# Optimization experiments

Measured on AMD Instinct MI355X. Metric: run time of the kernel, lower is better.

The kernel has to match this reference:

```python
import jax, jax.numpy as jnp
import numpy as np

N_NODES = 100000
N_EDGES = 1600000
D = 128
LEAKY_ALPHA = 0.2
ELU_ALPHA = 1.0


def setup_inputs() -> dict:
    key = jax.random.key(0)
    ks = jax.random.split(key, 8)
    s = 0.05
    atom_features = jax.random.normal(ks[0], (N_NODES, D), dtype=jnp.float32)
    W1 = jax.random.normal(ks[1], (1, 2 * D), dtype=jnp.float32) * s
    b1 = jnp.zeros((1,), dtype=jnp.float32)
    W2 = jax.random.normal(ks[2], (D, D), dtype=jnp.float32) * s
    b2 = jnp.zeros((D,), dtype=jnp.float32)
    w_ih = jax.random.normal(ks[3], (3 * D, D), dtype=jnp.float32) * s
    w_hh = jax.random.normal(ks[4], (3 * D, D), dtype=jnp.float32) * s
    b_ih = jnp.zeros((3 * D,), dtype=jnp.float32)
    b_hh = jnp.zeros((3 * D,), dtype=jnp.float32)
    edge_index = jax.random.randint(ks[5], (2, N_EDGES), 0, N_NODES, dtype=jnp.int64)
    return {"atom_features": atom_features, "W1": W1, "b1": b1, "W2": W2,
            "b2": b2, "w_ih": w_ih, "w_hh": w_hh, "b_ih": b_ih, "b_hh": b_hh,
            "edge_index": edge_index}


def _elu(x, alpha):
    return jnp.where(x > 0, x, alpha * (jnp.exp(jnp.minimum(x, 0.0)) - 1.0))


def reference(atom_features, W1, b1, W2, b2, w_ih, w_hh, b_ih, b_hh, edge_index):
    N, d = atom_features.shape
    src = edge_index[0]  # neighbor j (keys[0])
    dst = edge_index[1]  # center node i (keys[1])

    # atom_fc2 transform (dropout is identity in eval)
    nft = atom_features @ W2.T + b2  # [N, d]

    # attention logit per edge: leaky_relu(W1 @ concat(h_dst, h_src) + b1)
    w_d = W1[0, :d]
    w_s = W1[0, d:]
    logit = atom_features @ w_d  # [N]
    logit_src = atom_features @ w_s  # [N]
    score = logit[dst] + logit_src[src] + b1[0]  # [E]
    score = jnp.where(score > 0, score, LEAKY_ALPHA * score)

    # segment softmax over incoming edges of each dst node
    m = jax.ops.segment_max(score, dst, num_segments=N)  # -inf for isolated nodes
    m_safe = jnp.where(jnp.isfinite(m), m, 0.0)
    e = jnp.exp(score - m_safe[dst])  # [E]
    denom = jax.ops.segment_sum(e, dst, num_segments=N)  # [N]
    attn = e / denom[dst]  # [E]

    # weighted scatter-sum of transformed neighbor features
    msg = attn[:, None] * nft[src]  # [E, d]
    transform = jax.ops.segment_sum(msg, dst, num_segments=N)  # [N, d]
    context = _elu(transform, ELU_ALPHA)

    deg = jax.ops.segment_sum(jnp.ones_like(score), dst, num_segments=N)
    out_emb = jnp.where(deg[:, None] > 0, context, atom_features)

    # GRUCell(out_emb, atom_features): torch gate ordering r, z, n
    gi = out_emb @ w_ih.T + b_ih  # [N, 3d]
    gh = atom_features @ w_hh.T + b_hh  # [N, 3d]
    gi_r, gi_z, gi_n = jnp.split(gi, 3, axis=-1)
    gh_r, gh_z, gh_n = jnp.split(gh, 3, axis=-1)
    r = jax.nn.sigmoid(gi_r + gh_r)
    z = jax.nn.sigmoid(gi_z + gh_z)
    n = jnp.tanh(gi_n + r * gh_n)
    h_new = (1.0 - z) * n + z * atom_features
    return h_new
```

## Files before the change

kernel.cpp:

```cpp
#include <hip/hip_runtime.h>
#include <cstdint>
#include <cstddef>

#define D 128
#define LEAKY_ALPHA 0.2f

#define BSHIFT 8
#define BCAP 4608
#define NBUK_MAX 512

typedef __attribute__((ext_vector_type(8))) short short8;
typedef __attribute__((ext_vector_type(4))) short short4v;
typedef __attribute__((ext_vector_type(4))) float f32x4;
typedef __attribute__((ext_vector_type(2))) float f32x2;

static __device__ __forceinline__ unsigned short f32_to_bf16_rne(float v) {
  unsigned x = __float_as_uint(v);
  unsigned r = (x + 0x7fffu + ((x >> 16) & 1u)) >> 16;
  return (unsigned short)r;
}
static __device__ __forceinline__ float bf16_to_f32(unsigned short u) {
  return __uint_as_float(((unsigned)u) << 16);
}

#if __has_builtin(__builtin_amdgcn_cvt_pk_f32_fp8) && __has_builtin(__builtin_amdgcn_cvt_pk_fp8_f32)
#define FP8_HW 1
#endif

static __device__ __forceinline__ unsigned char f32_to_fp8(float x) {
#ifdef FP8_HW
  return (unsigned char)(__builtin_amdgcn_cvt_pk_fp8_f32(x, x, 0, false) & 0xff);
#else
  unsigned u = __float_as_uint(x);
  unsigned s = (u >> 24) & 0x80u;
  unsigned mag = u & 0x7fffffffu;
  if (mag == 0) return (unsigned char)s;
  int e = (int)(mag >> 23) - 127;
  unsigned full = (mag & 0x7fffffu) | 0x800000u;
  if (e >= 9) return (unsigned char)(s | 0x7Eu);
  int sh = (e >= -6) ? 20 : 20 + (-6 - e);
  if (sh > 24) return (unsigned char)s;
  unsigned keep = full >> sh;
  unsigned rem = full & ((1u << sh) - 1u);
  unsigned half = 1u << (sh - 1);
  if (rem > half || (rem == half && (keep & 1u))) keep++;
  unsigned em;
  if (e >= -6) {
    unsigned v = ((unsigned)(e + 7) << 3) + keep - 8u;
    if (v > 0x7Eu) v = 0x7Eu;
    em = v;
  } else {
    em = keep;
  }
  return (unsigned char)(s | em);
#endif
}

#ifndef FP8_HW
static __device__ __forceinline__ float fp8_dec(unsigned b) {
  unsigned em = b & 0x7fu, s = (b & 0x80u) << 24;
  float m;
  if (em >= 8) m = __uint_as_float(0x3C000000u + (em << 20));
  else m = (float)em * 0.001953125f;
  return __uint_as_float(s | __float_as_uint(m));
}
#endif

static __device__ __forceinline__ void fp8_fma16(uint4 u, float e, float* acc) {
#ifdef FP8_HW
  f32x2 t;
  t = __builtin_amdgcn_cvt_pk_f32_fp8(u.x, false); acc[0] += e*t[0]; acc[1] += e*t[1];
  t = __builtin_amdgcn_cvt_pk_f32_fp8(u.x, true ); acc[2] += e*t[0]; acc[3] += e*t[1];
  t = __builtin_amdgcn_cvt_pk_f32_fp8(u.y, false); acc[4] += e*t[0]; acc[5] += e*t[1];
  t = __builtin_amdgcn_cvt_pk_f32_fp8(u.y, true ); acc[6] += e*t[0]; acc[7] += e*t[1];
  t = __builtin_amdgcn_cvt_pk_f32_fp8(u.z, false); acc[8] += e*t[0]; acc[9] += e*t[1];
  t = __builtin_amdgcn_cvt_pk_f32_fp8(u.z, true ); acc[10]+= e*t[0]; acc[11]+= e*t[1];
  t = __builtin_amdgcn_cvt_pk_f32_fp8(u.w, false); acc[12]+= e*t[0]; acc[13]+= e*t[1];
  t = __builtin_amdgcn_cvt_pk_f32_fp8(u.w, true ); acc[14]+= e*t[0]; acc[15]+= e*t[1];
#else
  unsigned ws[4] = {u.x, u.y, u.z, u.w};
  #pragma unroll
  for (int k = 0; k < 4; ++k)
    #pragma unroll
    for (int b = 0; b < 4; ++b)
      acc[k * 4 + b] += e * fp8_dec((ws[k] >> (8 * b)) & 0xffu);
#endif
}

__global__ __launch_bounds__(256) void k_wprep(
    const float* __restrict__ W1, const float* __restrict__ W2,
    const float* __restrict__ w_ih, const float* __restrict__ w_hh,
    unsigned short* __restrict__ Wcat, unsigned short* __restrict__ Wb) {
  int idx = blockIdx.x * 256 + threadIdx.x;
  if (idx < 144 * 128) {
    int r = idx >> 7, c = idx & 127;
    float v = 0.f;
    if (r < 128)      v = W2[r * 128 + c];
    else if (r == 128) v = W1[c];
    else if (r == 129) v = W1[128 + c];
    Wcat[idx] = f32_to_bf16_rne(v);
    return;
  }
  int i2 = idx - 144 * 128;
  if (i2 < 384 * 256) {
    int r = i2 >> 8, c = i2 & 255;
    float v = (c < D) ? w_ih[r * D + c] : w_hh[r * D + (c - D)];
    Wb[i2] = f32_to_bf16_rne(v);
  }
}

#define NPITCH 136
__global__ __launch_bounds__(256, 2) void k_front(
    const float* __restrict__ A, const unsigned short* __restrict__ Wcat,
    const float* __restrict__ b2, unsigned char* __restrict__ nftb,
    float* __restrict__ logit_d, float* __restrict__ logit_s,
    unsigned short* __restrict__ X,
    const int* __restrict__ ei, unsigned* __restrict__ cursors,
    unsigned* __restrict__ part,
    int N, int E, int NBUK, int EPB, int nftBlocks) {
  __shared__ short sA[64 * NPITCH];
  __shared__ int hist[NBUK_MAX];
  __shared__ int sbase[NBUK_MAX];
  int tid = threadIdx.x;

  if ((int)blockIdx.x >= nftBlocks) {
    int t = tid;
    int pb = blockIdx.x - nftBlocks;
    int e0 = pb * EPB;
    int e1 = min(e0 + EPB, E);
    for (int i = t; i < NBUK; i += 256) hist[i] = 0;
    __syncthreads();
    for (int e = e0 + t; e < e1; e += 256)
      atomicAdd(&hist[ei[E + e] >> BSHIFT], 1);
    __syncthreads();
    for (int i = t; i < NBUK; i += 256) {
      int h = hist[i];
      sbase[i] = h ? (int)atomicAdd(&cursors[i * 16], (unsigned)h) : 0;
      hist[i] = 0;
    }
    __syncthreads();
    for (int e = e0 + t; e < e1; e += 256) {
      int src = ei[e];
      int dst = ei[E + e];
      int b = dst >> BSHIFT;
      int lp = sbase[b] + atomicAdd(&hist[b], 1);
      if (lp < BCAP)
        part[(size_t)b * BCAP + lp] =
            ((unsigned)(dst & ((1 << BSHIFT) - 1)) << 24) | (unsigned)src;
    }
    return;
  }

  int n0 = blockIdx.x * 64;

  #pragma unroll
  for (int i = 0; i < 8; ++i) {
    int g = i * 1024 + tid * 4;
    int row = g >> 7, col = g & 127;
    int gr = n0 + row; if (gr >= N) gr = N - 1;
    float4 v = *(const float4*)&A[(size_t)gr * D + col];
    short4v b;
    b.x = (short)f32_to_bf16_rne(v.x);
    b.y = (short)f32_to_bf16_rne(v.y);
    b.z = (short)f32_to_bf16_rne(v.z);
    b.w = (short)f32_to_bf16_rne(v.w);
    *(short4v*)&sA[row * NPITCH + col] = b;
  }
  __syncthreads();

  int w = tid >> 6, lane = tid & 63, l15 = lane & 15, l4 = lane >> 4;

  f32x4 acc[4][2], acc8[4];
  #pragma unroll
  for (int rt = 0; rt < 4; ++rt) {
    acc[rt][0] = (f32x4)0.f; acc[rt][1] = (f32x4)0.f; acc8[rt] = (f32x4)0.f;
  }

  #pragma unroll
  for (int ks = 0; ks < 4; ++ks) {
    int kk = ks * 32 + l4 * 8;
    short8 a[4];
    #pragma unroll
    for (int rt = 0; rt < 4; ++rt)
      a[rt] = *(const short8*)&sA[(rt * 16 + l15) * NPITCH + kk];
    short8 b0 = *(const short8*)&Wcat[(size_t)(w * 16 + l15) * 128 + kk];
    short8 b1 = *(const short8*)&Wcat[(size_t)((w + 4) * 16 + l15) * 128 + kk];
    #pragma unroll
    for (int rt = 0; rt < 4; ++rt) {
      acc[rt][0] = __builtin_amdgcn_mfma_f32_16x16x32_bf16(a[rt], b0, acc[rt][0], 0, 0, 0);
      acc[rt][1] = __builtin_amdgcn_mfma_f32_16x16x32_bf16(a[rt], b1, acc[rt][1], 0, 0, 0);
    }
    if (w == 0) {
      short8 b2v = *(const short8*)&Wcat[(size_t)(128 + l15) * 128 + kk];
      #pragma unroll
      for (int rt = 0; rt < 4; ++rt)
        acc8[rt] = __builtin_amdgcn_mfma_f32_16x16x32_bf16(a[rt], b2v, acc8[rt], 0, 0, 0);
    }
  }

  #pragma unroll
  for (int i = 0; i < 4; ++i) {
    int g = i * 2048 + tid * 8;
    int row = g >> 7, col = g & 127;
    if (n0 + row < N) {
      short8 v = *(const short8*)&sA[row * NPITCH + col];
      *(short8*)&X[(size_t)(n0 + row) * 256 + 128 + col] = v;
    }
  }

  #pragma unroll
  for (int t = 0; t < 2; ++t) {
    int j = (w + 4 * t) * 16 + l15;
    float bb = b2[j];
    #pragma unroll
    for (int rt = 0; rt < 4; ++rt)
      #pragma unroll
      for (int jr = 0; jr < 4; ++jr) {
        int row = n0 + rt * 16 + l4 * 4 + jr;
        if (row < N)
          nftb[(size_t)row * D + j] = f32_to_fp8(acc[rt][t][jr] + bb);
      }
  }
  if (w == 0 && l15 < 2) {
    float* dst = (l15 == 0) ? logit_d : logit_s;
    #pragma unroll
    for (int rt = 0; rt < 4; ++rt)
      #pragma unroll
      for (int jr = 0; jr < 4; ++jr) {
        int row = n0 + rt * 16 + l4 * 4 + jr;
        if (row < N) dst[row] = acc8[rt][jr];
      }
  }
}

__global__ __launch_bounds__(256) void k_bucket_csr(
    const unsigned* __restrict__ cursors, const unsigned* __restrict__ part,
    const float* __restrict__ logit_d, const float* __restrict__ logit_s,
    const float* __restrict__ b1, uint2* __restrict__ rec,
    int2* __restrict__ beg_end, int N) {
  __shared__ unsigned ents[BCAP];
  __shared__ int hist[256];
  __shared__ int scn[256];
  __shared__ int cur[256];
  __shared__ float sld[256];
  int b = blockIdx.x, t = threadIdx.x;
  int nb0 = b << BSHIFT;
  int cnt = (int)cursors[b * 16];
  if (cnt > BCAP) cnt = BCAP;
  hist[t] = 0;
  {
    int n = nb0 + t;
    sld[t] = (n < N) ? logit_d[n] + b1[0] : 0.f;
  }
  __syncthreads();
  const unsigned* reg = part + (size_t)b * BCAP;
  uint2* rrec = rec + (size_t)b * BCAP;
  for (int i = t; i < cnt; i += 256) {
    unsigned p = reg[i];
    ents[i] = p;
    atomicAdd(&hist[p >> 24], 1);
  }
  __syncthreads();
  int v = hist[t];
  scn[t] = v;
  __syncthreads();
  for (int o = 1; o < 256; o <<= 1) {
    int x = (t >= o) ? scn[t - o] : 0;
    __syncthreads();
    scn[t] += x;
    __syncthreads();
  }
  int excl = scn[t] - v;
  cur[t] = excl;
  int n = nb0 + t;
  if (n < N) beg_end[n] = make_int2(b * BCAP + excl, b * BCAP + excl + v);
  __syncthreads();
  for (int i = t; i < cnt; i += 256) {
    unsigned p = ents[i];
    int dl = p >> 24;
    int lp = atomicAdd(&cur[dl], 1);
    unsigned s = p & 0xFFFFFFu;
    float sc = sld[dl] + logit_s[s];
    sc = sc > 0.f ? sc : LEAKY_ALPHA * sc;
    rrec[lp] = make_uint2(s, __float_as_uint(__expf(sc)));
  }
}

#define XPITCH 264
__global__ __launch_bounds__(512, 1) void k_gat_gru(
    const int2* __restrict__ beg_end, const uint2* __restrict__ rec,
    const unsigned char* __restrict__ nftb,
    const unsigned short* X,
    const unsigned short* __restrict__ Wb,
    const float* __restrict__ b_ih, const float* __restrict__ b_hh,
    float* out, int N) {
  __shared__ short sX[64 * XPITCH];
  int tid = threadIdx.x;
  int n0 = blockIdx.x * 64;

  #pragma unroll
  for (int i = 0; i < 2; ++i) {
    int idx = i * 512 + tid;
    int row = idx >> 4, c8 = idx & 15;
    int gr = n0 + row; if (gr >= N) gr = N - 1;
    short8 v = *(const short8*)&X[(size_t)gr * 256 + 128 + c8 * 8];
    *(short8*)&sX[row * XPITCH + 128 + c8 * 8] = v;
  }
  __syncthreads();

  {
    int l  = tid & 7;
    int nl = tid >> 3;
    int n  = n0 + nl;
    short8 xo0, xo1;
    if (n < N) {
      int2 be = beg_end[n];
      int start = be.x, end = be.y;
      if (end == start) {
        xo0 = *(const short8*)&sX[nl * XPITCH + 128 + l * 16];
        xo1 = *(const short8*)&sX[nl * XPITCH + 128 + l * 16 + 8];
      } else {
        float acc[16];
        #pragma unroll
        for (int j = 0; j < 16; ++j) acc[j] = 0.f;
        float den = 0.f;
        int p = start;
        for (; p + 4 <= end; p += 4) {
          uint2 r0 = rec[p], r1 = rec[p + 1], r2 = rec[p + 2], r3 = rec[p + 3];
          uint4 u0 = *(const uint4*)&nftb[(size_t)r0.x * D + l * 16];
          uint4 u1 = *(const uint4*)&nftb[(size_t)r1.x * D + l * 16];
          uint4 u2 = *(const uint4*)&nftb[(size_t)r2.x * D + l * 16];
          uint4 u3 = *(const uint4*)&nftb[(size_t)r3.x * D + l * 16];
          float w0 = __uint_as_float(r0.y), w1 = __uint_as_float(r1.y);
          float w2 = __uint_as_float(r2.y), w3 = __uint_as_float(r3.y);
          den += (w0 + w1) + (w2 + w3);
          fp8_fma16(u0, w0, acc);
          fp8_fma16(u1, w1, acc);
          fp8_fma16(u2, w2, acc);
          fp8_fma16(u3, w3, acc);
        }
        for (; p < end; ++p) {
          uint2 r = rec[p];
          uint4 u = *(const uint4*)&nftb[(size_t)r.x * D + l * 16];
          float w0 = __uint_as_float(r.y);
          den += w0;
          fp8_fma16(u, w0, acc);
        }
        float inv = 1.f / den;
        #pragma unroll
        for (int j = 0; j < 16; ++j) {
          float t = acc[j] * inv;
          float oe = t > 0.f ? t : (__expf(t) - 1.f);
          if (j < 8) xo0[j] = (short)f32_to_bf16_rne(oe);
          else       xo1[j - 8] = (short)f32_to_bf16_rne(oe);
        }
      }
    } else {
      xo0 = (short8)0; xo1 = (short8)0;
    }
    *(short8*)&sX[nl * XPITCH + l * 16]     = xo0;
    *(short8*)&sX[nl * XPITCH + l * 16 + 8] = xo1;
  }
  __syncthreads();

  int w    = tid >> 6;
  int lane = tid & 63;
  int l15  = lane & 15;
  int l4   = lane >> 4;
  int j    = w * 16 + l15;

  f32x4 acc[4][4];
  #pragma unroll
  for (int rt = 0; rt < 4; ++rt)
    #pragma unroll
    for (int q = 0; q < 4; ++q) acc[rt][q] = (f32x4)0.f;

  #pragma unroll
  for (int ks = 0; ks < 8; ++ks) {
    int kk = ks * 32 + l4 * 8;
    short8 a[4];
    #pragma unroll
    for (int rt = 0; rt < 4; ++rt)
      a[rt] = *(const short8*)&sX[(rt * 16 + l15) * XPITCH + kk];
    short8 b0 = *(const short8*)&Wb[(size_t)(j) * 256 + kk];
    short8 b1 = *(const short8*)&Wb[(size_t)(128 + j) * 256 + kk];
    short8 b2 = *(const short8*)&Wb[(size_t)(256 + j) * 256 + kk];
    int qn = (ks < 4) ? 2 : 3;
    #pragma unroll
    for (int rt = 0; rt < 4; ++rt) {
      acc[rt][0]  = __builtin_amdgcn_mfma_f32_16x16x32_bf16(a[rt], b0, acc[rt][0], 0, 0, 0);
      acc[rt][1]  = __builtin_amdgcn_mfma_f32_16x16x32_bf16(a[rt], b1, acc[rt][1], 0, 0, 0);
      acc[rt][qn] = __builtin_amdgcn_mfma_f32_16x16x32_bf16(a[rt], b2, acc[rt][qn], 0, 0, 0);
    }
  }

  float br  = b_ih[j] + b_hh[j];
  float bz  = b_ih[D + j] + b_hh[D + j];
  float bin = b_ih[2 * D + j];
  float bhn = b_hh[2 * D + j];
  #pragma unroll
  for (int rt = 0; rt < 4; ++rt) {
    #pragma unroll
    for (int jr = 0; jr < 4; ++jr) {
      int lrow = rt * 16 + l4 * 4 + jr;
      int row = n0 + lrow;
      if (row < N) {
        float rp  = acc[rt][0][jr] + br;
        float zp  = acc[rt][1][jr] + bz;
        float gin = acc[rt][2][jr] + bin;
        float ghn = acc[rt][3][jr] + bhn;
        float r = 1.f / (1.f + __expf(-rp));
        float z = 1.f / (1.f + __expf(-zp));
        float t = gin + r * ghn;
        float e2 = __expf(2.f * t);
        float nn = 1.f - 2.f / (e2 + 1.f);
        float h = bf16_to_f32((unsigned short)sX[lrow * XPITCH + 128 + j]);
        out[(size_t)row * D + j] = (1.f - z) * nn + z * h;
      }
    }
  }
}

extern "C" void kernel_launch(void* const* d_in, const int* in_sizes, int n_in,
                              void* d_out, int out_size, void* d_ws, size_t ws_size,
                              hipStream_t stream) {
  const float* A    = (const float*)d_in[0];
  const float* W1   = (const float*)d_in[1];
  const float* b1   = (const float*)d_in[2];
  const float* W2   = (const float*)d_in[3];
  const float* b2   = (const float*)d_in[4];
  const float* w_ih = (const float*)d_in[5];
  const float* w_hh = (const float*)d_in[6];
  const float* b_ih = (const float*)d_in[7];
  const float* b_hh = (const float*)d_in[8];
  const int*   ei   = (const int*)d_in[9];

  int N = in_sizes[0] / D;
  int E = in_sizes[9] / 2;
  float* out = (float*)d_out;

  int NBUK = (N + (1 << BSHIFT) - 1) >> BSHIFT;

  char* ws = (char*)d_ws;
  unsigned char* nftb = (unsigned char*)ws;
  float* logit_d = (float*)(ws + (size_t)N * D);
  float* logit_s = logit_d + N;
  int2*  beg_end = (int2*)(logit_s + N);
  unsigned* cursors = (unsigned*)(beg_end + N);
  unsigned* part = cursors + (size_t)NBUK * 16;
  uint2* rec = (uint2*)(part + (size_t)NBUK * BCAP);
  unsigned short* Wb   = (unsigned short*)(rec + (size_t)NBUK * BCAP);
  unsigned short* Wcat = Wb + 384 * 256;

  hipMemsetAsync(cursors, 0, (size_t)NBUK * 16 * sizeof(unsigned), stream);

  k_wprep<<<(144 * 128 + 384 * 256 + 255) / 256, 256, 0, stream>>>(
      W1, W2, w_ih, w_hh, Wcat, Wb);

  int nftBlocks = (N + 63) / 64;
  int gridPart = 160;
  int EPB = (E + gridPart - 1) / gridPart;
  k_front<<<nftBlocks + gridPart, 256, 0, stream>>>(
      A, Wcat, b2, nftb, logit_d, logit_s, (unsigned short*)d_out,
      ei, cursors, part, N, E, NBUK, EPB, nftBlocks);

  k_bucket_csr<<<NBUK, 256, 0, stream>>>(cursors, part, logit_d, logit_s, b1,
                                         rec, beg_end, N);
  k_gat_gru<<<nftBlocks, 512, 0, stream>>>(beg_end, rec, nftb,
                                           (const unsigned short*)d_out,
                                           Wb, b_ih, b_hh, out, N);
}
```

Baseline: 191.8 us.

## Fuse bucket CSR build into GAT/GRU kernel with 64-node buckets

```diff
diff --git a/kernel.cpp b/kernel.cpp
--- a/kernel.cpp
+++ b/kernel.cpp
@@ -5,9 +5,9 @@
 #define D 128
 #define LEAKY_ALPHA 0.2f
 
-#define BSHIFT 8
-#define BCAP 4608
-#define NBUK_MAX 512
+#define BSHIFT 6
+#define BCAP 1344
+#define NBUK_MAX 2048
 
 typedef __attribute__((ext_vector_type(8))) short short8;
 typedef __attribute__((ext_vector_type(4))) short short4v;
@@ -90,7 +90,8 @@
 __global__ __launch_bounds__(256) void k_wprep(
     const float* __restrict__ W1, const float* __restrict__ W2,
     const float* __restrict__ w_ih, const float* __restrict__ w_hh,
-    unsigned short* __restrict__ Wcat, unsigned short* __restrict__ Wb) {
+    unsigned short* __restrict__ Wcat, unsigned short* __restrict__ Wb,
+    unsigned* __restrict__ cursors, int ncur) {
   int idx = blockIdx.x * 256 + threadIdx.x;
   if (idx < 144 * 128) {
     int r = idx >> 7, c = idx & 127;
@@ -106,7 +107,10 @@
     int r = i2 >> 8, c = i2 & 255;
     float v = (c < D) ? w_ih[r * D + c] : w_hh[r * D + (c - D)];
     Wb[i2] = f32_to_bf16_rne(v);
-  }
+    return;
+  }
+  int i3 = i2 - 384 * 256;
+  if (i3 < ncur) cursors[i3] = 0;
 }
 
 #define NPITCH 136
@@ -233,70 +237,27 @@
   }
 }
 
-__global__ __launch_bounds__(256) void k_bucket_csr(
+#define XPITCH 264
+__global__ __launch_bounds__(512, 1) void k_gat_gru(
     const unsigned* __restrict__ cursors, const unsigned* __restrict__ part,
     const float* __restrict__ logit_d, const float* __restrict__ logit_s,
-    const float* __restrict__ b1, uint2* __restrict__ rec,
-    int2* __restrict__ beg_end, int N) {
-  __shared__ unsigned ents[BCAP];
-  __shared__ int hist[256];
-  __shared__ int scn[256];
-  __shared__ int cur[256];
-  __shared__ float sld[256];
-  int b = blockIdx.x, t = threadIdx.x;
-  int nb0 = b << BSHIFT;
-  int cnt = (int)cursors[b * 16];
-  if (cnt > BCAP) cnt = BCAP;
-  hist[t] = 0;
-  {
-    int n = nb0 + t;
-    sld[t] = (n < N) ? logit_d[n] + b1[0] : 0.f;
-  }
-  __syncthreads();
-  const unsigned* reg = part + (size_t)b * BCAP;
-  uint2* rrec = rec + (size_t)b * BCAP;
-  for (int i = t; i < cnt; i += 256) {
-    unsigned p = reg[i];
-    ents[i] = p;
-    atomicAdd(&hist[p >> 24], 1);
-  }
-  __syncthreads();
-  int v = hist[t];
-  scn[t] = v;
-  __syncthreads();
-  for (int o = 1; o < 256; o <<= 1) {
-    int x = (t >= o) ? scn[t - o] : 0;
-    __syncthreads();
-    scn[t] += x;
-    __syncthreads();
-  }
-  int excl = scn[t] - v;
-  cur[t] = excl;
-  int n = nb0 + t;
-  if (n < N) beg_end[n] = make_int2(b * BCAP + excl, b * BCAP + excl + v);
-  __syncthreads();
-  for (int i = t; i < cnt; i += 256) {
-    unsigned p = ents[i];
-    int dl = p >> 24;
-    int lp = atomicAdd(&cur[dl], 1);
-    unsigned s = p & 0xFFFFFFu;
-    float sc = sld[dl] + logit_s[s];
-    sc = sc > 0.f ? sc : LEAKY_ALPHA * sc;
-    rrec[lp] = make_uint2(s, __float_as_uint(__expf(sc)));
-  }
-}
-
-#define XPITCH 264
-__global__ __launch_bounds__(512, 1) void k_gat_gru(
-    const int2* __restrict__ beg_end, const uint2* __restrict__ rec,
+    const float* __restrict__ b1,
     const unsigned char* __restrict__ nftb,
     const unsigned short* X,
     const unsigned short* __restrict__ Wb,
     const float* __restrict__ b_ih, const float* __restrict__ b_hh,
     float* out, int N) {
   __shared__ short sX[64 * XPITCH];
+  __shared__ unsigned ents[BCAP];
+  __shared__ uint2 srec[BCAP];
+  __shared__ int sbeg[64], scnt[64], cur[64];
+  __shared__ float sld[64];
   int tid = threadIdx.x;
-  int n0 = blockIdx.x * 64;
+  int b   = blockIdx.x;
+  int n0  = b * 64;
+
+  int cnt = (int)cursors[b * 16];
+  if (cnt > BCAP) cnt = BCAP;
 
   #pragma unroll
   for (int i = 0; i < 2; ++i) {
@@ -306,6 +267,41 @@
     short8 v = *(const short8*)&X[(size_t)gr * 256 + 128 + c8 * 8];
     *(short8*)&sX[row * XPITCH + 128 + c8 * 8] = v;
   }
+  for (int i = tid; i < cnt; i += 512) ents[i] = part[(size_t)b * BCAP + i];
+  if (tid < 64) {
+    int n = n0 + tid;
+    sld[tid] = (n < N) ? logit_d[n] + b1[0] : 0.f;
+    scnt[tid] = 0;
+  }
+  __syncthreads();
+
+  for (int i = tid; i < cnt; i += 512)
+    atomicAdd(&scnt[ents[i] >> 24], 1);
+  __syncthreads();
+
+  if (tid < 64) {
+    int v = scnt[tid];
+    int incl = v;
+    #pragma unroll
+    for (int o = 1; o < 64; o <<= 1) {
+      int x = __shfl_up(incl, o);
+      if (tid >= o) incl += x;
+    }
+    int excl = incl - v;
+    sbeg[tid] = excl;
+    cur[tid]  = excl;
+  }
+  __syncthreads();
+
+  for (int i = tid; i < cnt; i += 512) {
+    unsigned p = ents[i];
+    int dl = p >> 24;
+    unsigned s = p & 0xFFFFFFu;
+    int lp = atomicAdd(&cur[dl], 1);
+    float sc = sld[dl] + logit_s[s];
+    sc = sc > 0.f ? sc : LEAKY_ALPHA * sc;
+    srec[lp] = make_uint2(s, __float_as_uint(__expf(sc)));
+  }
   __syncthreads();
 
   {
@@ -314,8 +310,8 @@
     int n  = n0 + nl;
     short8 xo0, xo1;
     if (n < N) {
-      int2 be = beg_end[n];
-      int start = be.x, end = be.y;
+      int start = sbeg[nl];
+      int end   = start + scnt[nl];
       if (end == start) {
         xo0 = *(const short8*)&sX[nl * XPITCH + 128 + l * 16];
         xo1 = *(const short8*)&sX[nl * XPITCH + 128 + l * 16 + 8];
@@ -326,7 +322,7 @@
         float den = 0.f;
         int p = start;
         for (; p + 4 <= end; p += 4) {
-          uint2 r0 = rec[p], r1 = rec[p + 1], r2 = rec[p + 2], r3 = rec[p + 3];
+          uint2 r0 = srec[p], r1 = srec[p + 1], r2 = srec[p + 2], r3 = srec[p + 3];
           uint4 u0 = *(const uint4*)&nftb[(size_t)r0.x * D + l * 16];
           uint4 u1 = *(const uint4*)&nftb[(size_t)r1.x * D + l * 16];
           uint4 u2 = *(const uint4*)&nftb[(size_t)r2.x * D + l * 16];
@@ -340,7 +336,7 @@
           fp8_fma16(u3, w3, acc);
         }
         for (; p < end; ++p) {
-          uint2 r = rec[p];
+          uint2 r = srec[p];
           uint4 u = *(const uint4*)&nftb[(size_t)r.x * D + l * 16];
           float w0 = __uint_as_float(r.y);
           den += w0;
@@ -445,17 +441,15 @@
   unsigned char* nftb = (unsigned char*)ws;
   float* logit_d = (float*)(ws + (size_t)N * D);
   float* logit_s = logit_d + N;
-  int2*  beg_end = (int2*)(logit_s + N);
-  unsigned* cursors = (unsigned*)(beg_end + N);
+  unsigned* cursors = (unsigned*)(logit_s + N);
   unsigned* part = cursors + (size_t)NBUK * 16;
-  uint2* rec = (uint2*)(part + (size_t)NBUK * BCAP);
-  unsigned short* Wb   = (unsigned short*)(rec + (size_t)NBUK * BCAP);
+  unsigned short* Wb   = (unsigned short*)(part + (size_t)NBUK * BCAP);
   unsigned short* Wcat = Wb + 384 * 256;
 
-  hipMemsetAsync(cursors, 0, (size_t)NBUK * 16 * sizeof(unsigned), stream);
-
-  k_wprep<<<(144 * 128 + 384 * 256 + 255) / 256, 256, 0, stream>>>(
-      W1, W2, w_ih, w_hh, Wcat, Wb);
+  int ncur = NBUK * 16;
+  int wprepWork = 144 * 128 + 384 * 256 + ncur;
+  k_wprep<<<(wprepWork + 255) / 256, 256, 0, stream>>>(
+      W1, W2, w_ih, w_hh, Wcat, Wb, cursors, ncur);
 
   int nftBlocks = (N + 63) / 64;
   int gridPart = 160;
@@ -464,9 +458,7 @@
       A, Wcat, b2, nftb, logit_d, logit_s, (unsigned short*)d_out,
       ei, cursors, part, N, E, NBUK, EPB, nftBlocks);
 
-  k_bucket_csr<<<NBUK, 256, 0, stream>>>(cursors, part, logit_d, logit_s, b1,
-                                         rec, beg_end, N);
-  k_gat_gru<<<nftBlocks, 512, 0, stream>>>(beg_end, rec, nftb,
-                                           (const unsigned short*)d_out,
+  k_gat_gru<<<nftBlocks, 512, 0, stream>>>(cursors, part, logit_d, logit_s, b1,
+                                           nftb, (const unsigned short*)d_out,
                                            Wb, b_ih, b_hh, out, N);
 }
```

New measurement: 191.5 us. No clear change (-0.1%).
